# Kernel tuning notes

Hardware: AMD Instinct MI355X
Metric: run time of the kernel (lower is better)

## Reference

```python
import jax, jax.numpy as jnp
import numpy as np

B, S, T, D = 16, 512, 16, 128
LN_EPS = 1e-5


def setup_inputs() -> dict:
    key = jax.random.key(0)
    k_x, k_h, k_w = jax.random.split(key, 3)
    x = jax.random.normal(k_x, (B, S, T, D), dtype=jnp.float32)
    # prev_hidden must be strictly positive (code takes its log)
    prev_hidden = jax.random.uniform(k_h, (B, 1, T, D), dtype=jnp.float32) * 0.9 + 0.05
    ln_gamma = jnp.ones((D,), jnp.float32)
    ln_beta = jnp.zeros((D,), jnp.float32)
    # torch Linear(dim, 2*dim): store as (D, 2D) for x @ W
    W = jax.random.normal(k_w, (D, 2 * D), dtype=jnp.float32) * (1.0 / np.sqrt(D))
    b = jnp.zeros((2 * D,), jnp.float32)
    return {"x": x, "prev_hidden": prev_hidden, "ln_gamma": ln_gamma,
            "ln_beta": ln_beta, "W": W, "b": b}


def _g_act_log(h):
    # log of G activation: x>=0 -> log(relu(x)+0.5); x<0 -> -softplus(-x)
    return jnp.where(h >= 0, jnp.log(jax.nn.relu(h) + 0.5), -jax.nn.softplus(-h))


def reference(x, prev_hidden, ln_gamma, ln_beta, W, b):
    seq_len = x.shape[1]
    # LayerNorm over last dim
    mu = jnp.mean(x, axis=-1, keepdims=True)
    var = jnp.var(x, axis=-1, keepdims=True)
    xn = (x - mu) * jax.lax.rsqrt(var + LN_EPS) * ln_gamma + ln_beta
    gh = jnp.einsum('bstd,de->bste', xn, W) + b  # (B,S,T,2D)
    gate, hidden = jnp.split(gh, 2, axis=-1)
    # parallel (seq_len > 1) log-space path
    log_coeffs = -jax.nn.softplus(gate)          # log(1 - z)
    log_z = -jax.nn.softplus(-gate)              # log z
    log_values = log_z + _g_act_log(hidden)      # (B,S,T,D)
    # prepend prev_hidden: values get log(h0), coeffs get zero pad
    log_values = jnp.concatenate([jnp.log(prev_hidden), log_values], axis=1)
    zero_pad = jnp.zeros_like(log_coeffs[:, :1])
    log_coeffs = jnp.concatenate([zero_pad, log_coeffs], axis=1)
    # Heinsen associative scan in log space
    a_star = jnp.cumsum(log_coeffs, axis=1)
    log_h0_plus_b_star = jax.lax.cumlogsumexp(log_values - a_star, axis=1)
    out = jnp.exp(a_star + log_h0_plus_b_star)
    out = out[:, -seq_len:]
    next_prev_hidden = out[:, -1:]
    return out, next_prev_hidden
```

## Files before the change

### kernel.cpp

```cpp
#include <hip/hip_runtime.h>
#include <hip/hip_bf16.h>
#include <stdint.h>

#define BB 16
#define SS 512
#define TT 16
#define DD 128
#define CH 64
#define NCH (SS/CH)
#define LN_EPS 1e-5f

typedef __attribute__((ext_vector_type(8))) short short8;
typedef __attribute__((ext_vector_type(4))) float f32x4;

static __device__ __forceinline__ uint32_t cvt_pk_bf16(float lo, float hi) {
    uint32_t r;
    asm("v_cvt_pk_bf16_f32 %0, %1, %2" : "=v"(r) : "v"(lo), "v"(hi));
    return r;
}

#define BAR() do {                                            \
    asm volatile("s_waitcnt lgkmcnt(0)" ::: "memory");        \
    __builtin_amdgcn_s_barrier();                             \
    asm volatile("" ::: "memory");                            \
} while (0)

__global__ __launch_bounds__(512, 2) void fused_mingru(
    const float* __restrict__ x, const float* __restrict__ prevh,
    const float* __restrict__ gamma, const float* __restrict__ beta,
    const float* __restrict__ W, const float* __restrict__ bias,
    float* __restrict__ out, float* __restrict__ nexth)
{
    __shared__ __align__(16) unsigned char xnb[2][CH*256];

    const int tid  = threadIdx.x;
    const int w    = tid >> 6;
    const int lane = tid & 63;
    const int l15  = lane & 15;
    const int lhi  = lane >> 4;

    const int bt = blockIdx.x;
    const size_t rowstride = (size_t)TT * DD;
    const size_t base_bt   = ((size_t)(bt >> 4) * SS * TT + (bt & 15)) * DD;

    const int r_ln  = tid >> 3;
    const int c8    = tid & 7;
    const int rx_ln = r_ln & 7;
    const float* xp0 = x + base_bt + (size_t)r_ln * rowstride + c8*16;

    f32x4 px0, px1, px2, px3;
    auto issuePx = [&](int st) {
        const float* xp = xp0 + (size_t)st * CH * rowstride;
        px0 = *(const f32x4*)(xp + 0);
        px1 = *(const f32x4*)(xp + 4);
        px2 = *(const f32x4*)(xp + 8);
        px3 = *(const f32x4*)(xp + 12);
    };
    issuePx(0);

    short8 wfr[2][4];
    float  bs2[2];
    #pragma unroll
    for (int ni = 0; ni < 2; ++ni) {
        const int col = (ni ? 128 : 0) + w*16 + l15;
        float acc = 0.0f;
        #pragma unroll
        for (int kt = 0; kt < 4; ++kt) {
            union { short8 s8; uint32_t u[4]; } fr;
            #pragma unroll
            for (int p = 0; p < 4; ++p) {
                const int k0 = kt*32 + lhi*8 + 2*p;
                const float w0 = W[(size_t)k0*256 + col];
                const float w1 = W[(size_t)(k0+1)*256 + col];
                acc = fmaf(beta[k0],   w0, acc);
                acc = fmaf(beta[k0+1], w1, acc);
                fr.u[p] = cvt_pk_bf16(gamma[k0]*w0, gamma[k0+1]*w1);
            }
            wfr[ni][kt] = fr.s8;
        }
        acc += __shfl_xor(acc, 16);
        acc += __shfl_xor(acc, 32);
        bs2[ni] = bias[col] + acc;
    }

    float hM = prevh[(size_t)bt*128 + w*16 + l15];

    auto phaseLN = [&](int st) {
        float s1 = px0.x+px0.y+px0.z+px0.w + px1.x+px1.y+px1.z+px1.w
                 + px2.x+px2.y+px2.z+px2.w + px3.x+px3.y+px3.z+px3.w;
        float s2 = px0.x*px0.x+px0.y*px0.y+px0.z*px0.z+px0.w*px0.w
                 + px1.x*px1.x+px1.y*px1.y+px1.z*px1.z+px1.w*px1.w
                 + px2.x*px2.x+px2.y*px2.y+px2.z*px2.z+px2.w*px2.w
                 + px3.x*px3.x+px3.y*px3.y+px3.z*px3.z+px3.w*px3.w;
        s1 += __shfl_xor(s1, 1); s2 += __shfl_xor(s2, 1);
        s1 += __shfl_xor(s1, 2); s2 += __shfl_xor(s2, 2);
        s1 += __shfl_xor(s1, 4); s2 += __shfl_xor(s2, 4);
        const float mu = s1 * (1.0f/128.0f);
        const float rs = rsqrtf(s2 * (1.0f/128.0f) - mu*mu + LN_EPS);
        unsigned char* row = xnb[st & 1] + r_ln*256;
        union { short8 s8; uint32_t u[4]; } a, b2;
        a.u[0]  = cvt_pk_bf16((px0.x-mu)*rs, (px0.y-mu)*rs);
        a.u[1]  = cvt_pk_bf16((px0.z-mu)*rs, (px0.w-mu)*rs);
        a.u[2]  = cvt_pk_bf16((px1.x-mu)*rs, (px1.y-mu)*rs);
        a.u[3]  = cvt_pk_bf16((px1.z-mu)*rs, (px1.w-mu)*rs);
        b2.u[0] = cvt_pk_bf16((px2.x-mu)*rs, (px2.y-mu)*rs);
        b2.u[1] = cvt_pk_bf16((px2.z-mu)*rs, (px2.w-mu)*rs);
        b2.u[2] = cvt_pk_bf16((px3.x-mu)*rs, (px3.y-mu)*rs);
        b2.u[3] = cvt_pk_bf16((px3.z-mu)*rs, (px3.w-mu)*rs);
        *(short8*)(row + (((2*c8)     ^ rx_ln) << 4)) = a.s8;
        *(short8*)(row + (((2*c8 + 1) ^ rx_ln) << 4)) = b2.s8;
    };

    auto phaseG = [&](int st) {
        const unsigned char* xb = xnb[st & 1];
        #pragma unroll
        for (int mt = 0; mt < 4; ++mt) {
            const unsigned char* rowp = xb + (mt*16 + l15)*256;
            short8 af[4];
            #pragma unroll
            for (int kt = 0; kt < 4; ++kt) {
                const int c = (kt << 2) | lhi;
                af[kt] = *(const short8*)(rowp + ((c ^ (l15 & 7)) << 4));
            }
            f32x4 ag = (f32x4)(0.f), ah = (f32x4)(0.f);
            #pragma unroll
            for (int kt = 0; kt < 4; ++kt) {
                ag = __builtin_amdgcn_mfma_f32_16x16x32_bf16(af[kt], wfr[0][kt], ag, 0, 0, 0);
                ah = __builtin_amdgcn_mfma_f32_16x16x32_bf16(af[kt], wfr[1][kt], ah, 0, 0, 0);
            }
            float Lc[4], Lv[4];
            #pragma unroll
            for (int j = 0; j < 4; ++j) {
                const float g  = ag[j] + bs2[0];
                const float hh = ah[j] + bs2[1];
                const float cc = 1.0f / (1.0f + __expf(g));
                const float ga = (hh >= 0.0f) ? (hh + 0.5f)
                                              : (1.0f / (1.0f + __expf(-hh)));
                const float vv = (1.0f - cc) * ga;
                if (j == 0) { Lc[0] = cc; Lv[0] = vv; }
                else        { Lc[j] = cc * Lc[j-1]; Lv[j] = fmaf(cc, Lv[j-1], vv); }
            }
            float Ic = Lc[3], Iv = Lv[3];
            float pc = __shfl_up(Ic, 16), pv = __shfl_up(Iv, 16);
            if (lhi >= 1) { Iv = fmaf(Ic, pv, Iv); Ic *= pc; }
            pc = __shfl_up(Ic, 32); pv = __shfl_up(Iv, 32);
            if (lhi >= 2) { Iv = fmaf(Ic, pv, Iv); Ic *= pc; }
            float Ec = __shfl_up(Ic, 16), Ev = __shfl_up(Iv, 16);
            if (lhi == 0) { Ec = 1.0f; Ev = 0.0f; }
            const float Mc = __shfl(Ic, 48 + l15);
            const float Mv = __shfl(Iv, 48 + l15);
            const float hE = fmaf(Ec, hM, Ev);
            float* op = out + base_bt
                      + (size_t)(st*CH + mt*16 + lhi*4) * rowstride + w*16 + l15;
            #pragma unroll
            for (int j = 0; j < 4; ++j)
                op[(size_t)j * rowstride] = fmaf(Lc[j], hE, Lv[j]);
            hM = fmaf(Mc, hM, Mv);
        }
    };

    phaseLN(0);
    issuePx(1);
    BAR();

    for (int st = 0; st < NCH; ++st) {
        phaseG(st);
        if (st + 1 < NCH) {
            phaseLN(st + 1);
            if (st + 2 < NCH) issuePx(st + 2);
        }
        BAR();
    }

    if (lane < 16)
        nexth[(size_t)bt*128 + w*16 + lane] = hM;
}

extern "C" void kernel_launch(void* const* d_in, const int* in_sizes, int n_in,
                              void* d_out, int out_size, void* d_ws, size_t ws_size,
                              hipStream_t stream) {
    const float* x     = (const float*)d_in[0];
    const float* prevh = (const float*)d_in[1];
    const float* gamma = (const float*)d_in[2];
    const float* beta  = (const float*)d_in[3];
    const float* W     = (const float*)d_in[4];
    const float* bias  = (const float*)d_in[5];

    float* out   = (float*)d_out;
    float* nexth = out + (size_t)BB*SS*TT*DD;

    fused_mingru<<<BB*TT, 512, 0, stream>>>(x, prevh, gamma, beta, W, bias,
                                            out, nexth);
}
```

Measured before the change: 42.91 us.

## Permute LDS row layout so each lane scans 16 contiguous timesteps per chunk

LayerNorm rows are written to a permuted LDS slot so that, after the four MFMA tiles, each lane holds 16 consecutive timesteps of the chunk instead of 4 per tile. The serial recurrence now runs 16 steps in registers, followed by one cross-lane shuffle scan per 64-step chunk instead of four. This cuts the shuffle and carry work in the scan but holds more registers live (32 extra floats) and changes the output store pattern.

```diff
diff --git a/kernel.cpp b/kernel.cpp
--- a/kernel.cpp
+++ b/kernel.cpp
@@ -43,9 +43,10 @@
     const size_t rowstride = (size_t)TT * DD;
     const size_t base_bt   = ((size_t)(bt >> 4) * SS * TT + (bt & 15)) * DD;
 
-    const int r_ln  = tid >> 3;
-    const int c8    = tid & 7;
-    const int rx_ln = r_ln & 7;
+    const int r_ln = tid >> 3;
+    const int c8   = tid & 7;
+    const int slot_p = ((r_ln >> 2) & 3)*16 + (r_ln >> 4)*4 + (r_ln & 3);
+    const int keyx   = slot_p & 7;
     const float* xp0 = x + base_bt + (size_t)r_ln * rowstride + c8*16;
 
     f32x4 px0, px1, px2, px3;
@@ -97,7 +98,7 @@
         s1 += __shfl_xor(s1, 4); s2 += __shfl_xor(s2, 4);
         const float mu = s1 * (1.0f/128.0f);
         const float rs = rsqrtf(s2 * (1.0f/128.0f) - mu*mu + LN_EPS);
-        unsigned char* row = xnb[st & 1] + r_ln*256;
+        unsigned char* row = xnb[st & 1] + slot_p*256;
         union { short8 s8; uint32_t u[4]; } a, b2;
         a.u[0]  = cvt_pk_bf16((px0.x-mu)*rs, (px0.y-mu)*rs);
         a.u[1]  = cvt_pk_bf16((px0.z-mu)*rs, (px0.w-mu)*rs);
@@ -107,12 +108,13 @@
         b2.u[1] = cvt_pk_bf16((px2.z-mu)*rs, (px2.w-mu)*rs);
         b2.u[2] = cvt_pk_bf16((px3.x-mu)*rs, (px3.y-mu)*rs);
         b2.u[3] = cvt_pk_bf16((px3.z-mu)*rs, (px3.w-mu)*rs);
-        *(short8*)(row + (((2*c8)     ^ rx_ln) << 4)) = a.s8;
-        *(short8*)(row + (((2*c8 + 1) ^ rx_ln) << 4)) = b2.s8;
+        *(short8*)(row + (((2*c8)     ^ keyx) << 4)) = a.s8;
+        *(short8*)(row + (((2*c8 + 1) ^ keyx) << 4)) = b2.s8;
     };
 
     auto phaseG = [&](int st) {
         const unsigned char* xb = xnb[st & 1];
+        float Cc[16], Cv[16];
         #pragma unroll
         for (int mt = 0; mt < 4; ++mt) {
             const unsigned char* rowp = xb + (mt*16 + l15)*256;
@@ -128,7 +130,6 @@
                 ag = __builtin_amdgcn_mfma_f32_16x16x32_bf16(af[kt], wfr[0][kt], ag, 0, 0, 0);
                 ah = __builtin_amdgcn_mfma_f32_16x16x32_bf16(af[kt], wfr[1][kt], ah, 0, 0, 0);
             }
-            float Lc[4], Lv[4];
             #pragma unroll
             for (int j = 0; j < 4; ++j) {
                 const float g  = ag[j] + bs2[0];
@@ -136,27 +137,30 @@
                 const float cc = 1.0f / (1.0f + __expf(g));
                 const float ga = (hh >= 0.0f) ? (hh + 0.5f)
                                               : (1.0f / (1.0f + __expf(-hh)));
-                const float vv = (1.0f - cc) * ga;
-                if (j == 0) { Lc[0] = cc; Lv[0] = vv; }
-                else        { Lc[j] = cc * Lc[j-1]; Lv[j] = fmaf(cc, Lv[j-1], vv); }
+                Cc[mt*4 + j] = cc;
+                Cv[mt*4 + j] = (1.0f - cc) * ga;
             }
-            float Ic = Lc[3], Iv = Lv[3];
-            float pc = __shfl_up(Ic, 16), pv = __shfl_up(Iv, 16);
-            if (lhi >= 1) { Iv = fmaf(Ic, pv, Iv); Ic *= pc; }
-            pc = __shfl_up(Ic, 32); pv = __shfl_up(Iv, 32);
-            if (lhi >= 2) { Iv = fmaf(Ic, pv, Iv); Ic *= pc; }
-            float Ec = __shfl_up(Ic, 16), Ev = __shfl_up(Iv, 16);
-            if (lhi == 0) { Ec = 1.0f; Ev = 0.0f; }
-            const float Mc = __shfl(Ic, 48 + l15);
-            const float Mv = __shfl(Iv, 48 + l15);
-            const float hE = fmaf(Ec, hM, Ev);
-            float* op = out + base_bt
-                      + (size_t)(st*CH + mt*16 + lhi*4) * rowstride + w*16 + l15;
-            #pragma unroll
-            for (int j = 0; j < 4; ++j)
-                op[(size_t)j * rowstride] = fmaf(Lc[j], hE, Lv[j]);
-            hM = fmaf(Mc, hM, Mv);
         }
+        #pragma unroll
+        for (int i = 1; i < 16; ++i) {
+            Cv[i] = fmaf(Cc[i], Cv[i-1], Cv[i]);
+            Cc[i] = Cc[i] * Cc[i-1];
+        }
+        float Ic = Cc[15], Iv = Cv[15];
+        float pc = __shfl_up(Ic, 16), pv = __shfl_up(Iv, 16);
+        if (lhi >= 1) { Iv = fmaf(Ic, pv, Iv); Ic *= pc; }
+        pc = __shfl_up(Ic, 32); pv = __shfl_up(Iv, 32);
+        if (lhi >= 2) { Iv = fmaf(Ic, pv, Iv); Ic *= pc; }
+        float Ec = __shfl_up(Ic, 16), Ev = __shfl_up(Iv, 16);
+        if (lhi == 0) { Ec = 1.0f; Ev = 0.0f; }
+        const float Mc = __shfl(Ic, 48 + l15);
+        const float Mv = __shfl(Iv, 48 + l15);
+        const float hE = fmaf(Ec, hM, Ev);
+        float* op = out + base_bt + (size_t)(st*CH + lhi*16) * rowstride + w*16 + l15;
+        #pragma unroll
+        for (int i = 0; i < 16; ++i)
+            op[(size_t)i * rowstride] = fmaf(Cc[i], hE, Cv[i]);
+        hM = fmaf(Mc, hM, Mv);
     };
 
     phaseLN(0);
```

Result: faster. 41.93 us (-2.3%).
